# Kernel tuning notes

Measured on AMD Instinct MI355X. Metric: run time of the kernel, lower is better.

Reference implementation:

```python
import jax, jax.numpy as jnp
import numpy as np

MAX_DEG = 10  # PyG MFConv default max_degree


def mfconv(x, edge_index, W, b, Wr):
    """Degree-bucketed graph conv (PyG MFConv).
    x: [N, F_in]; edge_index: [2, E]; W, Wr: [MAX_DEG+1, F_in, F_out]; b: [MAX_DEG+1, F_out].
    out_i = lins[deg_i](sum_{j in N(i)} x_j) + root_lins[deg_i](x_i)
    """
    N = x.shape[0]
    src, dst = edge_index[0], edge_index[1]
    # sum-aggregate neighbor features (gather + scatter-add)
    h = jax.ops.segment_sum(x[src], dst, num_segments=N)  # [N, F_in]
    # in-degree per node, clamped to MAX_DEG
    deg = jax.ops.segment_sum(jnp.ones_like(dst, dtype=jnp.int32), dst, num_segments=N)
    deg = jnp.clip(deg, 0, MAX_DEG)  # [N]
    # compute all degree-bucket outputs, then select per node ([N, D+1, F_out] is small)
    out_all = jnp.einsum('nf,dfo->ndo', h, W) + b[None] + jnp.einsum('nf,dfo->ndo', x, Wr)
    return jnp.take_along_axis(out_all, deg[:, None, None], axis=1)[:, 0]  # [N, F_out]


def setup_inputs() -> dict:
    key = jax.random.key(0)
    ks = jax.random.split(key, 8)
    N, E = 100000, 1600000
    F_in, F_hid, F_out = 128, 32, 64
    D = MAX_DEG + 1
    x = jax.random.normal(ks[0], (N, F_in), dtype=jnp.float32)
    edge_index = jax.random.randint(ks[1], (2, E), 0, N, dtype=jnp.int64)
    s1 = 1.0 / np.sqrt(F_in)
    s2 = 1.0 / np.sqrt(F_hid)
    W1 = jax.random.uniform(ks[2], (D, F_in, F_hid), jnp.float32, -s1, s1)
    b1 = jax.random.uniform(ks[3], (D, F_hid), jnp.float32, -s1, s1)
    Wr1 = jax.random.uniform(ks[4], (D, F_in, F_hid), jnp.float32, -s1, s1)
    W2 = jax.random.uniform(ks[5], (D, F_hid, F_out), jnp.float32, -s2, s2)
    b2 = jax.random.uniform(ks[6], (D, F_out), jnp.float32, -s2, s2)
    Wr2 = jax.random.uniform(ks[7], (D, F_hid, F_out), jnp.float32, -s2, s2)
    return {"x": x, "edge_index": edge_index, "W1": W1, "b1": b1, "Wr1": Wr1,
            "W2": W2, "b2": b2, "Wr2": Wr2}


def reference(x, edge_index, W1, b1, Wr1, W2, b2, Wr2):
    h = mfconv(x, edge_index, W1, b1, Wr1)
    h = jax.nn.relu(h)
    return mfconv(h, edge_index, W2, b2, Wr2)
```

## Files before the change

kernel.cpp:

```cpp
#include <hip/hip_runtime.h>

#define FIN 128
#define FHID 32
#define FOUT 64
#define MAXDEG 10
#define BSH 8
#define ACHUNK 4096
#define XPAD 136
#define YPAD 40

typedef __attribute__((ext_vector_type(8))) short short8;
typedef __attribute__((ext_vector_type(4))) float f32x4;


__device__ __forceinline__ float bf2f(unsigned short u) {
    union { unsigned int i; float f; } c; c.i = ((unsigned int)u) << 16; return c.f;
}
__device__ __forceinline__ unsigned short f2bf(float f) {
    union { float f; unsigned int i; } c; c.f = f;
    unsigned int r = c.i + 0x7FFF + ((c.i >> 16) & 1);
    return (unsigned short)(r >> 16);
}
__device__ __forceinline__ float bflo(unsigned int w) { return bf2f((unsigned short)(w & 0xffff)); }
__device__ __forceinline__ float bfhi(unsigned int w) { return bf2f((unsigned short)(w >> 16)); }
__device__ __forceinline__ unsigned int pk2(float lo, float hi) {
    return (unsigned int)f2bf(lo) | ((unsigned int)f2bf(hi) << 16);
}


__global__ __launch_bounds__(256) void k_bhist(const int* __restrict__ ei, int E, int N,
                                               int* __restrict__ bcnt) {
    __shared__ int hist[1024];
    int K = ((N + 255) >> BSH);
    int t = threadIdx.x;
    long long cb = (long long)blockIdx.x * ACHUNK;
    for (int i = t; i < K; i += 256) hist[i] = 0;
    __syncthreads();
#pragma unroll
    for (int i = 0; i < 16; ++i) {
        long long e = cb + t + (long long)i * 256;
        if (e < E) {
            int ss = ei[e];
            int dd = ei[E + e];
            if ((unsigned)ss < (unsigned)N && (unsigned)dd < (unsigned)N)
                atomicAdd(&hist[dd >> BSH], 1);
        }
    }
    __syncthreads();
    for (int i = t; i < K; i += 256) {
        int h = hist[i];
        if (h) atomicAdd(&bcnt[i], h);
    }
}

__global__ __launch_bounds__(1024) void k_scanb(const int* __restrict__ bcnt, int K,
                                                int* __restrict__ bstart,
                                                int* __restrict__ gcur) {
    __shared__ int tmp[1024];
    int t = threadIdx.x;
    int v = (t < K) ? bcnt[t] : 0;
    tmp[t] = v;
    __syncthreads();
    for (int off = 1; off < 1024; off <<= 1) {
        int a = (t >= off) ? tmp[t - off] : 0;
        __syncthreads();
        tmp[t] += a;
        __syncthreads();
    }
    if (t < K) { int s = tmp[t] - v; bstart[t] = s; gcur[t] = s; }
}

__global__ __launch_bounds__(256) void k_passA(const int* __restrict__ ei, int E, int N,
                                               int* __restrict__ gcur,
                                               int2* __restrict__ pairs) {
    __shared__ int hist[1024];
    __shared__ int base[1024];
    int K = ((N + 255) >> BSH);
    int t = threadIdx.x;
    long long cb = (long long)blockIdx.x * ACHUNK;
    for (int i = t; i < K; i += 256) hist[i] = 0;
    __syncthreads();
    int sv[16], dv[16];
#pragma unroll
    for (int i = 0; i < 16; ++i) {
        sv[i] = -1; dv[i] = 0;
        long long e = cb + t + (long long)i * 256;
        if (e < E) {
            int ss = ei[e];
            int dd = ei[E + e];
            if ((unsigned)ss < (unsigned)N && (unsigned)dd < (unsigned)N) {
                sv[i] = ss; dv[i] = dd;
            }
        }
    }
#pragma unroll
    for (int i = 0; i < 16; ++i)
        if (sv[i] >= 0) atomicAdd(&hist[dv[i] >> BSH], 1);
    __syncthreads();
    for (int i = t; i < K; i += 256) {
        int h = hist[i];
        base[i] = h ? atomicAdd(&gcur[i], h) : 0;
    }
    __syncthreads();
    for (int i = t; i < K; i += 256) hist[i] = 0;
    __syncthreads();
#pragma unroll
    for (int i = 0; i < 16; ++i) {
        if (sv[i] >= 0) {
            int b = dv[i] >> BSH;
            int off = atomicAdd(&hist[b], 1);
            pairs[base[b] + off] = make_int2(sv[i], dv[i]);
        }
    }
}

__global__ __launch_bounds__(256) void k_passB2(const int2* __restrict__ pairs,
                                                const int* __restrict__ bstart,
                                                const int* __restrict__ gcur,
                                                int* __restrict__ deg,
                                                int* __restrict__ cursor,
                                                int* __restrict__ adj,
                                                int* __restrict__ nflag,
                                                int* __restrict__ flist, int N) {
    __shared__ int cnt[256];
    __shared__ int scn[256];
    __shared__ int cur[256];
    __shared__ int fids[256];
    __shared__ int fcnt, fbase;
    int b = blockIdx.x;
    int lo = b << BSH;
    int t = threadIdx.x;
    int nvalid = min(256, N - lo);
    cnt[t] = 0;
    if (t == 0) fcnt = 0;
    int pstart = bstart[b];
    int pend = gcur[b];
    __syncthreads();
    for (int i = pstart + t; i < pend; i += 256)
        atomicAdd(&cnt[pairs[i].y - lo], 1);
    __syncthreads();
    int v = cnt[t];
    scn[t] = v;
    __syncthreads();
    for (int off = 1; off < 256; off <<= 1) {
        int a = (t >= off) ? scn[t - off] : 0;
        __syncthreads();
        scn[t] += a;
        __syncthreads();
    }
    int rowstart = pstart + scn[t] - v;
    cur[t] = rowstart;
    if (t < nvalid) {
        deg[lo + t] = v;
        cursor[lo + t] = rowstart + v;
        if (v < MAXDEG) { int p = atomicAdd(&fcnt, 1); fids[p] = lo + t; }
    }
    __syncthreads();
    if (t == 0 && fcnt > 0) fbase = atomicAdd(nflag, fcnt);
    __syncthreads();
    if (t < fcnt) flist[fbase + t] = fids[t];
    for (int i = pstart + t; i < pend; i += 256) {
        int2 pr = pairs[i];
        int pos = atomicAdd(&cur[pr.y - lo], 1);
        adj[pos] = pr.x;
    }
}

__global__ __launch_bounds__(256) void k_prepack(const float* __restrict__ W1,
                                                 const float* __restrict__ Wr1,
                                                 const float* __restrict__ W2,
                                                 const float* __restrict__ Wr2,
                                                 unsigned short* __restrict__ wcat1,
                                                 unsigned short* __restrict__ wcat2) {
    int t = threadIdx.x;
    const float* W1b  = W1  + (size_t)MAXDEG * FIN * FHID;
    const float* Wr1b = Wr1 + (size_t)MAXDEG * FIN * FHID;
    const float* W2b  = W2  + (size_t)MAXDEG * FHID * FOUT;
    const float* Wr2b = Wr2 + (size_t)MAXDEG * FHID * FOUT;
    for (int i = 0; i < 32; ++i) {
        int idx = i * 256 + t;
        int n = idx >> 7, k = idx & 127;
        float v = (n < 32) ? W1b[k * FHID + n] : Wr1b[k * FHID + (n - 32)];
        wcat1[idx] = f2bf(v);
    }
    for (int i = 0; i < 16; ++i) {
        int idx = i * 256 + t;
        int n = idx >> 5, k = idx & 31;
        float v = (n < 64) ? W2b[k * FOUT + n] : Wr2b[k * FOUT + (n - 64)];
        wcat2[idx] = f2bf(v);
    }
}

__global__ __launch_bounds__(256) void k_pre1m(const float* __restrict__ x,
                                               const unsigned short* __restrict__ wcat1,
                                               const float* __restrict__ b1,
                                               unsigned short* __restrict__ z10,
                                               unsigned short* __restrict__ r1, int N) {
    __shared__ __align__(16) unsigned short xt[64 * XPAD];
    __shared__ __align__(16) unsigned short wt[64 * XPAD];
    int t = threadIdx.x;
    int row0 = blockIdx.x * 64;
    {
        const uint4* src = (const uint4*)wcat1;
#pragma unroll
        for (int i = 0; i < 4; ++i) {
            int idx = i * 256 + t;
            uint4 v = src[idx];
            int n = idx >> 4;
            int k = (idx & 15) * 8;
            *(uint4*)(wt + n * XPAD + k) = v;
        }
    }
    {
        int r = t >> 2;
        int c0 = (t & 3) * 32;
        int cr = min(row0 + r, N - 1);
        const float4* xs = (const float4*)(x + (size_t)cr * FIN + c0);
        unsigned short* dst = xt + r * XPAD + c0;
#pragma unroll
        for (int i = 0; i < 8; ++i) {
            float4 v = xs[i];
            ushort4 b;
            b.x = f2bf(v.x); b.y = f2bf(v.y); b.z = f2bf(v.z); b.w = f2bf(v.w);
            *(ushort4*)(dst + i * 4) = b;
        }
    }
    __syncthreads();
    int w = t >> 6, lane = t & 63;
    int m = lane & 15, quad = lane >> 4;
    const unsigned short* arow = xt + (w * 16 + m) * XPAD + quad * 8;
    short8 af[4];
#pragma unroll
    for (int kt = 0; kt < 4; ++kt) af[kt] = *(const short8*)(arow + kt * 32);
    f32x4 acc[4];
#pragma unroll
    for (int ct = 0; ct < 4; ++ct) acc[ct] = (f32x4){0.f, 0.f, 0.f, 0.f};
#pragma unroll
    for (int ct = 0; ct < 4; ++ct) {
        const unsigned short* brow = wt + (ct * 16 + m) * XPAD + quad * 8;
#pragma unroll
        for (int kt = 0; kt < 4; ++kt) {
            short8 bfr = *(const short8*)(brow + kt * 32);
            acc[ct] = __builtin_amdgcn_mfma_f32_16x16x32_bf16(af[kt], bfr, acc[ct], 0, 0, 0);
        }
    }
    int rbase = row0 + w * 16 + quad * 4;
#pragma unroll
    for (int ct = 0; ct < 4; ++ct) {
        float bias = (ct >= 2) ? b1[MAXDEG * FHID + (ct - 2) * 16 + m] : 0.f;
#pragma unroll
        for (int rg = 0; rg < 4; ++rg) {
            int n = rbase + rg;
            if (n < N) {
                float v = acc[ct][rg];
                if (ct < 2) z10[(size_t)n * FHID + ct * 16 + m] = f2bf(v);
                else        r1[(size_t)n * FHID + (ct - 2) * 16 + m] = f2bf(v + bias);
            }
        }
    }
}

__global__ __launch_bounds__(256) void k_fix1c(const float* __restrict__ x,
                                               const int* __restrict__ deg,
                                               const int* __restrict__ cursor,
                                               const int* __restrict__ adj,
                                               const float* __restrict__ W1,
                                               const float* __restrict__ b1,
                                               const float* __restrict__ Wr1,
                                               const int* __restrict__ nflag,
                                               const int* __restrict__ flist,
                                               unsigned short* __restrict__ out1, int N) {
    int wid = (blockIdx.x * 256 + threadIdx.x) >> 6;
    int nw = gridDim.x * 4;
    int lane = threadIdx.x & 63;
    int u = lane >> 5, o = lane & 31;
    int fcnt = *nflag;
    for (int i = wid; i < fcnt; i += nw) {
        int n = flist[i];
        int d = deg[n];
        const float* Wr = Wr1 + (size_t)d * (FIN * FHID) + o;
        const float4* xr = (const float4*)(x + (size_t)n * FIN);
        float racc = 0.f;
        for (int c = u * 16; c < u * 16 + 16; ++c) {
            float4 xv = xr[c];
            racc += xv.x * Wr[(c * 4 + 0) * FHID] + xv.y * Wr[(c * 4 + 1) * FHID]
                  + xv.z * Wr[(c * 4 + 2) * FHID] + xv.w * Wr[(c * 4 + 3) * FHID];
        }
        racc += __shfl_xor(racc, 32);
        int e1 = cursor[n];
        int e0 = e1 - d;
        float2 h = make_float2(0.f, 0.f);
        for (int k = e0; k < e1; ++k) {
            int s = adj[k];
            float2 v = *(const float2*)(x + (size_t)s * FIN + lane * 2);
            h.x += v.x; h.y += v.y;
        }
        const float* Wp = W1 + (size_t)d * (FIN * FHID) + o;
        float acc = 0.f;
        for (int f = u * 64; f < u * 64 + 64; ++f) {
            float hf = __shfl((f & 1) ? h.y : h.x, f >> 1);
            acc += hf * Wp[f * FHID];
        }
        acc += __shfl_xor(acc, 32);
        if (lane < 32) {
            float rv = racc + b1[d * FHID + o];
            out1[(size_t)n * FHID + o] = f2bf(fmaxf(acc + rv, 0.f));
        }
    }
}

__device__ __forceinline__ void gather16(const unsigned short* __restrict__ rows,
                                         const int* __restrict__ adj,
                                         int e0, int e1, int cnt, int lane,
                                         float& a0, float& a1) {
    int e = lane >> 4, f2 = lane & 15;
    int sidx = adj[min(e0 + lane, e1 - 1)];
    const unsigned short* rb = rows + f2 * 2;
    int nch = (cnt + 15) >> 4;
    for (int c = 0; c < nch; ++c) {
        int i0 = c * 16 + e;
        int i1 = i0 + 4, i2 = i0 + 8, i3 = i0 + 12;
        int s0 = __shfl(sidx, min(i0, cnt - 1));
        int s1 = __shfl(sidx, min(i1, cnt - 1));
        int s2 = __shfl(sidx, min(i2, cnt - 1));
        int s3 = __shfl(sidx, min(i3, cnt - 1));
        unsigned int w0 = *(const unsigned int*)(rb + (size_t)s0 * FHID);
        unsigned int w1 = *(const unsigned int*)(rb + (size_t)s1 * FHID);
        unsigned int w2 = *(const unsigned int*)(rb + (size_t)s2 * FHID);
        unsigned int w3 = *(const unsigned int*)(rb + (size_t)s3 * FHID);
        float c0 = (i0 < cnt) ? 1.f : 0.f;
        float c1 = (i1 < cnt) ? 1.f : 0.f;
        float c2 = (i2 < cnt) ? 1.f : 0.f;
        float c3 = (i3 < cnt) ? 1.f : 0.f;
        a0 = fmaf(c0, bflo(w0), a0); a1 = fmaf(c0, bfhi(w0), a1);
        a0 = fmaf(c1, bflo(w1), a0); a1 = fmaf(c1, bfhi(w1), a1);
        a0 = fmaf(c2, bflo(w2), a0); a1 = fmaf(c2, bfhi(w2), a1);
        a0 = fmaf(c3, bflo(w3), a0); a1 = fmaf(c3, bfhi(w3), a1);
    }
    for (int k = e0 + 64 + e; k < e1; k += 4) {
        int s = adj[k];
        unsigned int w = *(const unsigned int*)(rb + (size_t)s * FHID);
        a0 += bflo(w); a1 += bfhi(w);
    }
}

__global__ __launch_bounds__(256) void k_layer1b(const unsigned short* __restrict__ z10,
                                                 const unsigned short* __restrict__ r1,
                                                 const int* __restrict__ deg,
                                                 const int* __restrict__ cursor,
                                                 const int* __restrict__ adj,
                                                 unsigned short* __restrict__ out1, int N) {
    int wave = (int)(((long long)blockIdx.x * 256 + threadIdx.x) >> 6);
    if (wave >= N) return;
    int n = wave;
    int lane = threadIdx.x & 63;
    int dg = deg[n];
    if (dg < MAXDEG) return;
    int e1 = cursor[n];
    int e0 = e1 - dg;
    float a0 = 0.f, a1 = 0.f;
    gather16(z10, adj, e0, e1, min(dg, 64), lane, a0, a1);
    a0 += __shfl_xor(a0, 16); a1 += __shfl_xor(a1, 16);
    a0 += __shfl_xor(a0, 32); a1 += __shfl_xor(a1, 32);
    if (lane < 16) {
        int f2 = lane;
        unsigned int rv = *(const unsigned int*)(r1 + (size_t)n * FHID + f2 * 2);
        unsigned int w = pk2(fmaxf(a0 + bflo(rv), 0.f), fmaxf(a1 + bfhi(rv), 0.f));
        *(unsigned int*)(out1 + (size_t)n * FHID + f2 * 2) = w;
    }
}

__global__ __launch_bounds__(256) void k_layer2g(const unsigned short* __restrict__ y,
                                                 const int* __restrict__ deg,
                                                 const int* __restrict__ cursor,
                                                 const int* __restrict__ adj,
                                                 float* __restrict__ g, int N) {
    int wave = (int)(((long long)blockIdx.x * 256 + threadIdx.x) >> 6);
    if (wave >= N) return;
    int n = wave;
    int lane = threadIdx.x & 63;
    int dg = deg[n];
    float a0 = 0.f, a1 = 0.f;
    if (dg > 0) {
        int e1 = cursor[n];
        int e0 = e1 - dg;
        gather16(y, adj, e0, e1, min(dg, 64), lane, a0, a1);
        a0 += __shfl_xor(a0, 16); a1 += __shfl_xor(a1, 16);
        a0 += __shfl_xor(a0, 32); a1 += __shfl_xor(a1, 32);
    }
    if (lane < 16) {
        *(float2*)(g + (size_t)n * FHID + lane * 2) = make_float2(a0, a1);
    }
}

__global__ __launch_bounds__(256) void k_post2m(const float* __restrict__ g,
                                                const unsigned short* __restrict__ y,
                                                const unsigned short* __restrict__ wcat2,
                                                const float* __restrict__ b2,
                                                float* __restrict__ out, int N) {
    __shared__ __align__(16) unsigned short gt[64 * YPAD];
    __shared__ __align__(16) unsigned short yt[64 * YPAD];
    __shared__ __align__(16) unsigned short wt[128 * YPAD];
    int t = threadIdx.x;
    int row0 = blockIdx.x * 64;
    {
        const uint4* src = (const uint4*)wcat2;
#pragma unroll
        for (int i = 0; i < 2; ++i) {
            int idx = i * 256 + t;
            uint4 v = src[idx];
            int nn = idx >> 2;
            int k = (idx & 3) * 8;
            *(uint4*)(wt + nn * YPAD + k) = v;
        }
    }
    {
        int r = t >> 2, c0 = (t & 3) * 8;
        int rn = min(row0 + r, N - 1);
        const float4* gs = (const float4*)(g + (size_t)rn * FHID + c0);
        float4 v0 = gs[0], v1 = gs[1];
        ushort4 p0, p1;
        p0.x = f2bf(v0.x); p0.y = f2bf(v0.y); p0.z = f2bf(v0.z); p0.w = f2bf(v0.w);
        p1.x = f2bf(v1.x); p1.y = f2bf(v1.y); p1.z = f2bf(v1.z); p1.w = f2bf(v1.w);
        *(ushort4*)(gt + r * YPAD + c0) = p0;
        *(ushort4*)(gt + r * YPAD + c0 + 4) = p1;
        uint4 vy = *(const uint4*)(y + (size_t)rn * FHID + c0);
        *(uint4*)(yt + r * YPAD + c0) = vy;
    }
    __syncthreads();
    int w = t >> 6, lane = t & 63;
    int m = lane & 15, quad = lane >> 4;
    short8 ag = *(const short8*)(gt + (w * 16 + m) * YPAD + quad * 8);
    short8 ay = *(const short8*)(yt + (w * 16 + m) * YPAD + quad * 8);
    int rbase = row0 + w * 16 + quad * 4;
#pragma unroll
    for (int ct = 0; ct < 4; ++ct) {
        short8 bw = *(const short8*)(wt + (ct * 16 + m) * YPAD + quad * 8);
        short8 br = *(const short8*)(wt + ((64 + ct * 16) + m) * YPAD + quad * 8);
        f32x4 acc = (f32x4){0.f, 0.f, 0.f, 0.f};
        acc = __builtin_amdgcn_mfma_f32_16x16x32_bf16(ag, bw, acc, 0, 0, 0);
        acc = __builtin_amdgcn_mfma_f32_16x16x32_bf16(ay, br, acc, 0, 0, 0);
        int o = ct * 16 + m;
        float bias = b2[MAXDEG * FOUT + o];
#pragma unroll
        for (int rg = 0; rg < 4; ++rg) {
            int nn = rbase + rg;
            if (nn < N) out[(size_t)nn * FOUT + o] = acc[rg] + bias;
        }
    }
}

__global__ __launch_bounds__(256) void k_fix2c(const float* __restrict__ g,
                                               const unsigned short* __restrict__ y,
                                               const int* __restrict__ deg,
                                               const float* __restrict__ b2,
                                               const float* __restrict__ W2,
                                               const float* __restrict__ Wr2,
                                               const int* __restrict__ nflag,
                                               const int* __restrict__ flist,
                                               float* __restrict__ out, int N) {
    int wid = (blockIdx.x * 256 + threadIdx.x) >> 6;
    int nw = gridDim.x * 4;
    int lane = threadIdx.x & 63;
    int fcnt = *nflag;
    for (int i = wid; i < fcnt; i += nw) {
        int n = flist[i];
        int d = deg[n];
        const float* W2p  = W2  + (size_t)d * (FHID * FOUT) + lane;
        const float* Wr2p = Wr2 + (size_t)d * (FHID * FOUT) + lane;
        float2 gv = *(const float2*)(g + (size_t)n * FHID + (lane & 15) * 2);
        unsigned int yw = *(const unsigned int*)(y + (size_t)n * FHID + (lane & 15) * 2);
        float acc = b2[d * FOUT + lane];
#pragma unroll
        for (int q = 0; q < 16; ++q) {
            float g0 = __shfl(gv.x, q);
            float g1 = __shfl(gv.y, q);
            unsigned int yq = __shfl(yw, q);
            acc += g0 * W2p[(2 * q) * FOUT] + g1 * W2p[(2 * q + 1) * FOUT]
                 + bflo(yq) * Wr2p[(2 * q) * FOUT] + bfhi(yq) * Wr2p[(2 * q + 1) * FOUT];
        }
        out[(size_t)n * FOUT + lane] = acc;
    }
}

extern "C" void kernel_launch(void* const* d_in, const int* in_sizes, int n_in,
                              void* d_out, int out_size, void* d_ws, size_t ws_size,
                              hipStream_t stream) {
    const float* x   = (const float*)d_in[0];
    const int*   ei  = (const int*)d_in[1];
    const float* W1  = (const float*)d_in[2];
    const float* b1  = (const float*)d_in[3];
    const float* Wr1 = (const float*)d_in[4];
    const float* W2  = (const float*)d_in[5];
    const float* b2  = (const float*)d_in[6];
    const float* Wr2 = (const float*)d_in[7];

    int N = in_sizes[0] / FIN;
    int E = in_sizes[1] / 2;
    int K  = (N + 255) >> BSH;

    char* ws = (char*)d_ws;
    size_t off = 0;
    auto alloc = [&](size_t bytes) {
        void* ptr = ws + off;
        off += (bytes + 511) / 512 * 512;
        return ptr;
    };
    int* deg              = (int*)alloc((size_t)N * sizeof(int));
    int* cursor           = (int*)alloc((size_t)N * sizeof(int));
    int* bcnt             = (int*)alloc((size_t)(K + 1) * sizeof(int));
    int* nflag            = bcnt + K;
    int* bstart           = (int*)alloc((size_t)K * sizeof(int));
    int* gcur             = (int*)alloc((size_t)K * sizeof(int));
    int* flist            = (int*)alloc((size_t)N * sizeof(int));
    int* adj              = (int*)alloc((size_t)E * sizeof(int));
    unsigned short* z10   = (unsigned short*)alloc((size_t)N * FHID * 2);
    unsigned short* r1    = (unsigned short*)alloc((size_t)N * FHID * 2);
    unsigned short* out1  = (unsigned short*)alloc((size_t)N * FHID * 2);
    size_t pairsB = (size_t)E * sizeof(int2);
    size_t gB     = (size_t)N * FHID * sizeof(float);
    void* shared_region   = alloc(pairsB > gB ? pairsB : gB);
    float* g              = (float*)shared_region;
    int2* pairs           = (int2*)shared_region;
    unsigned short* wcat1 = (unsigned short*)alloc(64 * 128 * 2);
    unsigned short* wcat2 = (unsigned short*)alloc(128 * 32 * 2);

    float* out = (float*)d_out;

    hipMemsetAsync(bcnt, 0, (size_t)(K + 1) * sizeof(int), stream);

    int nwgA = (E + ACHUNK - 1) / ACHUNK;
    k_prepack<<<1, 256, 0, stream>>>(W1, Wr1, W2, Wr2, wcat1, wcat2);
    k_bhist<<<nwgA, 256, 0, stream>>>(ei, E, N, bcnt);
    k_scanb<<<1, 1024, 0, stream>>>(bcnt, K, bstart, gcur);
    k_passA<<<nwgA, 256, 0, stream>>>(ei, E, N, gcur, pairs);
    k_passB2<<<K, 256, 0, stream>>>(pairs, bstart, gcur, deg, cursor, adj, nflag, flist, N);

    int nb64 = (N + 63) / 64;
    int nb_node = (N + 3) / 4;
    int nbfix = 1024;

    k_pre1m<<<nb64, 256, 0, stream>>>(x, wcat1, b1, z10, r1, N);
    k_fix1c<<<nbfix, 256, 0, stream>>>(x, deg, cursor, adj, W1, b1, Wr1, nflag, flist, out1, N);
    k_layer1b<<<nb_node, 256, 0, stream>>>(z10, r1, deg, cursor, adj, out1, N);
    k_layer2g<<<nb_node, 256, 0, stream>>>(out1, deg, cursor, adj, g, N);
    k_post2m<<<nb64, 256, 0, stream>>>(g, out1, wcat2, b2, out, N);
    k_fix2c<<<nbfix, 256, 0, stream>>>(g, out1, deg, b2, W2, Wr2, nflag, flist, out, N);
}
```

Before: 294.2 us.

## Fuse fixup kernels into main layer kernels and pack edge pairs into 32 bits

Merges the weight prepack into the bucket-histogram kernel, and merges the low-degree fixup kernels into the layer-1 gather and layer-2 post kernels as extra blocks. This cuts the number of launches and lets both paths run concurrently. Edge pairs are packed into one 32-bit word (source index plus local destination offset), which halves the bytes written and read during the sort. The gather loop gains a fast path for full 16-edge chunks. The 20-bit source field caps N at about one million, and the layer-2 fixup now re-gathers neighbour rows instead of reading the precomputed g.

```diff
diff --git a/kernel.cpp b/kernel.cpp
--- a/kernel.cpp
+++ b/kernel.cpp
@@ -8,6 +8,7 @@
 #define ACHUNK 4096
 #define XPAD 136
 #define YPAD 40
+#define SRCBITS 20
 
 typedef __attribute__((ext_vector_type(8))) short short8;
 typedef __attribute__((ext_vector_type(4))) float f32x4;
@@ -28,8 +29,14 @@
 }
 
 
-__global__ __launch_bounds__(256) void k_bhist(const int* __restrict__ ei, int E, int N,
-                                               int* __restrict__ bcnt) {
+__global__ __launch_bounds__(256) void k_bhistp(const int* __restrict__ ei, int E, int N,
+                                                int* __restrict__ bcnt,
+                                                const float* __restrict__ W1,
+                                                const float* __restrict__ Wr1,
+                                                const float* __restrict__ W2,
+                                                const float* __restrict__ Wr2,
+                                                unsigned short* __restrict__ wcat1,
+                                                unsigned short* __restrict__ wcat2) {
     __shared__ int hist[1024];
     int K = ((N + 255) >> BSH);
     int t = threadIdx.x;
@@ -51,6 +58,24 @@
         int h = hist[i];
         if (h) atomicAdd(&bcnt[i], h);
     }
+    if (blockIdx.x == 0) {
+        const float* W1b  = W1  + (size_t)MAXDEG * FIN * FHID;
+        const float* Wr1b = Wr1 + (size_t)MAXDEG * FIN * FHID;
+        const float* W2b  = W2  + (size_t)MAXDEG * FHID * FOUT;
+        const float* Wr2b = Wr2 + (size_t)MAXDEG * FHID * FOUT;
+        for (int i = 0; i < 32; ++i) {
+            int idx = i * 256 + t;
+            int n = idx >> 7, k = idx & 127;
+            float v = (n < 32) ? W1b[k * FHID + n] : Wr1b[k * FHID + (n - 32)];
+            wcat1[idx] = f2bf(v);
+        }
+        for (int i = 0; i < 16; ++i) {
+            int idx = i * 256 + t;
+            int n = idx >> 5, k = idx & 31;
+            float v = (n < 64) ? W2b[k * FOUT + n] : Wr2b[k * FOUT + (n - 64)];
+            wcat2[idx] = f2bf(v);
+        }
+    }
 }
 
 __global__ __launch_bounds__(1024) void k_scanb(const int* __restrict__ bcnt, int K,
@@ -72,7 +97,7 @@
 
 __global__ __launch_bounds__(256) void k_passA(const int* __restrict__ ei, int E, int N,
                                                int* __restrict__ gcur,
-                                               int2* __restrict__ pairs) {
+                                               unsigned int* __restrict__ pairs) {
     __shared__ int hist[1024];
     __shared__ int base[1024];
     int K = ((N + 255) >> BSH);
@@ -109,12 +134,12 @@
         if (sv[i] >= 0) {
             int b = dv[i] >> BSH;
             int off = atomicAdd(&hist[b], 1);
-            pairs[base[b] + off] = make_int2(sv[i], dv[i]);
-        }
-    }
-}
-
-__global__ __launch_bounds__(256) void k_passB2(const int2* __restrict__ pairs,
+            pairs[base[b] + off] = (unsigned int)sv[i] | ((unsigned int)(dv[i] & 255) << SRCBITS);
+        }
+    }
+}
+
+__global__ __launch_bounds__(256) void k_passB2(const unsigned int* __restrict__ pairs,
                                                 const int* __restrict__ bstart,
                                                 const int* __restrict__ gcur,
                                                 int* __restrict__ deg,
@@ -137,7 +162,7 @@
     int pend = gcur[b];
     __syncthreads();
     for (int i = pstart + t; i < pend; i += 256)
-        atomicAdd(&cnt[pairs[i].y - lo], 1);
+        atomicAdd(&cnt[pairs[i] >> SRCBITS], 1);
     __syncthreads();
     int v = cnt[t];
     scn[t] = v;
@@ -160,34 +185,9 @@
     __syncthreads();
     if (t < fcnt) flist[fbase + t] = fids[t];
     for (int i = pstart + t; i < pend; i += 256) {
-        int2 pr = pairs[i];
-        int pos = atomicAdd(&cur[pr.y - lo], 1);
-        adj[pos] = pr.x;
-    }
-}
-
-__global__ __launch_bounds__(256) void k_prepack(const float* __restrict__ W1,
-                                                 const float* __restrict__ Wr1,
-                                                 const float* __restrict__ W2,
-                                                 const float* __restrict__ Wr2,
-                                                 unsigned short* __restrict__ wcat1,
-                                                 unsigned short* __restrict__ wcat2) {
-    int t = threadIdx.x;
-    const float* W1b  = W1  + (size_t)MAXDEG * FIN * FHID;
-    const float* Wr1b = Wr1 + (size_t)MAXDEG * FIN * FHID;
-    const float* W2b  = W2  + (size_t)MAXDEG * FHID * FOUT;
-    const float* Wr2b = Wr2 + (size_t)MAXDEG * FHID * FOUT;
-    for (int i = 0; i < 32; ++i) {
-        int idx = i * 256 + t;
-        int n = idx >> 7, k = idx & 127;
-        float v = (n < 32) ? W1b[k * FHID + n] : Wr1b[k * FHID + (n - 32)];
-        wcat1[idx] = f2bf(v);
-    }
-    for (int i = 0; i < 16; ++i) {
-        int idx = i * 256 + t;
-        int n = idx >> 5, k = idx & 31;
-        float v = (n < 64) ? W2b[k * FOUT + n] : Wr2b[k * FOUT + (n - 64)];
-        wcat2[idx] = f2bf(v);
+        unsigned int pr = pairs[i];
+        int pos = atomicAdd(&cur[pr >> SRCBITS], 1);
+        adj[pos] = (int)(pr & ((1u << SRCBITS) - 1));
     }
 }
 
@@ -260,55 +260,6 @@
     }
 }
 
-__global__ __launch_bounds__(256) void k_fix1c(const float* __restrict__ x,
-                                               const int* __restrict__ deg,
-                                               const int* __restrict__ cursor,
-                                               const int* __restrict__ adj,
-                                               const float* __restrict__ W1,
-                                               const float* __restrict__ b1,
-                                               const float* __restrict__ Wr1,
-                                               const int* __restrict__ nflag,
-                                               const int* __restrict__ flist,
-                                               unsigned short* __restrict__ out1, int N) {
-    int wid = (blockIdx.x * 256 + threadIdx.x) >> 6;
-    int nw = gridDim.x * 4;
-    int lane = threadIdx.x & 63;
-    int u = lane >> 5, o = lane & 31;
-    int fcnt = *nflag;
-    for (int i = wid; i < fcnt; i += nw) {
-        int n = flist[i];
-        int d = deg[n];
-        const float* Wr = Wr1 + (size_t)d * (FIN * FHID) + o;
-        const float4* xr = (const float4*)(x + (size_t)n * FIN);
-        float racc = 0.f;
-        for (int c = u * 16; c < u * 16 + 16; ++c) {
-            float4 xv = xr[c];
-            racc += xv.x * Wr[(c * 4 + 0) * FHID] + xv.y * Wr[(c * 4 + 1) * FHID]
-                  + xv.z * Wr[(c * 4 + 2) * FHID] + xv.w * Wr[(c * 4 + 3) * FHID];
-        }
-        racc += __shfl_xor(racc, 32);
-        int e1 = cursor[n];
-        int e0 = e1 - d;
-        float2 h = make_float2(0.f, 0.f);
-        for (int k = e0; k < e1; ++k) {
-            int s = adj[k];
-            float2 v = *(const float2*)(x + (size_t)s * FIN + lane * 2);
-            h.x += v.x; h.y += v.y;
-        }
-        const float* Wp = W1 + (size_t)d * (FIN * FHID) + o;
-        float acc = 0.f;
-        for (int f = u * 64; f < u * 64 + 64; ++f) {
-            float hf = __shfl((f & 1) ? h.y : h.x, f >> 1);
-            acc += hf * Wp[f * FHID];
-        }
-        acc += __shfl_xor(acc, 32);
-        if (lane < 32) {
-            float rv = racc + b1[d * FHID + o];
-            out1[(size_t)n * FHID + o] = f2bf(fmaxf(acc + rv, 0.f));
-        }
-    }
-}
-
 __device__ __forceinline__ void gather16(const unsigned short* __restrict__ rows,
                                          const int* __restrict__ adj,
                                          int e0, int e1, int cnt, int lane,
@@ -316,9 +267,24 @@
     int e = lane >> 4, f2 = lane & 15;
     int sidx = adj[min(e0 + lane, e1 - 1)];
     const unsigned short* rb = rows + f2 * 2;
-    int nch = (cnt + 15) >> 4;
-    for (int c = 0; c < nch; ++c) {
+    int nfull = cnt >> 4;
+    for (int c = 0; c < nfull; ++c) {
         int i0 = c * 16 + e;
+        int s0 = __shfl(sidx, i0);
+        int s1 = __shfl(sidx, i0 + 4);
+        int s2 = __shfl(sidx, i0 + 8);
+        int s3 = __shfl(sidx, i0 + 12);
+        unsigned int w0 = *(const unsigned int*)(rb + (size_t)s0 * FHID);
+        unsigned int w1 = *(const unsigned int*)(rb + (size_t)s1 * FHID);
+        unsigned int w2 = *(const unsigned int*)(rb + (size_t)s2 * FHID);
+        unsigned int w3 = *(const unsigned int*)(rb + (size_t)s3 * FHID);
+        a0 += bflo(w0); a1 += bfhi(w0);
+        a0 += bflo(w1); a1 += bfhi(w1);
+        a0 += bflo(w2); a1 += bfhi(w2);
+        a0 += bflo(w3); a1 += bfhi(w3);
+    }
+    if (cnt & 15) {
+        int i0 = nfull * 16 + e;
         int i1 = i0 + 4, i2 = i0 + 8, i3 = i0 + 12;
         int s0 = __shfl(sidx, min(i0, cnt - 1));
         int s1 = __shfl(sidx, min(i1, cnt - 1));
@@ -344,29 +310,74 @@
     }
 }
 
-__global__ __launch_bounds__(256) void k_layer1b(const unsigned short* __restrict__ z10,
+__global__ __launch_bounds__(256) void k_layer1x(const unsigned short* __restrict__ z10,
                                                  const unsigned short* __restrict__ r1,
                                                  const int* __restrict__ deg,
                                                  const int* __restrict__ cursor,
                                                  const int* __restrict__ adj,
-                                                 unsigned short* __restrict__ out1, int N) {
-    int wave = (int)(((long long)blockIdx.x * 256 + threadIdx.x) >> 6);
-    if (wave >= N) return;
-    int n = wave;
-    int lane = threadIdx.x & 63;
-    int dg = deg[n];
-    if (dg < MAXDEG) return;
-    int e1 = cursor[n];
-    int e0 = e1 - dg;
-    float a0 = 0.f, a1 = 0.f;
-    gather16(z10, adj, e0, e1, min(dg, 64), lane, a0, a1);
-    a0 += __shfl_xor(a0, 16); a1 += __shfl_xor(a1, 16);
-    a0 += __shfl_xor(a0, 32); a1 += __shfl_xor(a1, 32);
-    if (lane < 16) {
-        int f2 = lane;
-        unsigned int rv = *(const unsigned int*)(r1 + (size_t)n * FHID + f2 * 2);
-        unsigned int w = pk2(fmaxf(a0 + bflo(rv), 0.f), fmaxf(a1 + bfhi(rv), 0.f));
-        *(unsigned int*)(out1 + (size_t)n * FHID + f2 * 2) = w;
+                                                 const float* __restrict__ x,
+                                                 const float* __restrict__ W1,
+                                                 const float* __restrict__ b1,
+                                                 const float* __restrict__ Wr1,
+                                                 const int* __restrict__ nflag,
+                                                 const int* __restrict__ flist,
+                                                 unsigned short* __restrict__ out1,
+                                                 int N, int nbFast) {
+    int t = threadIdx.x;
+    int lane = t & 63;
+    if ((int)blockIdx.x < nbFast) {
+        int n = blockIdx.x * 4 + (t >> 6);
+        if (n >= N) return;
+        int dg = deg[n];
+        if (dg < MAXDEG) return;
+        int e1 = cursor[n];
+        int e0 = e1 - dg;
+        float a0 = 0.f, a1 = 0.f;
+        gather16(z10, adj, e0, e1, min(dg, 64), lane, a0, a1);
+        a0 += __shfl_xor(a0, 16); a1 += __shfl_xor(a1, 16);
+        a0 += __shfl_xor(a0, 32); a1 += __shfl_xor(a1, 32);
+        if (lane < 16) {
+            unsigned int rv = *(const unsigned int*)(r1 + (size_t)n * FHID + lane * 2);
+            unsigned int w = pk2(fmaxf(a0 + bflo(rv), 0.f), fmaxf(a1 + bfhi(rv), 0.f));
+            *(unsigned int*)(out1 + (size_t)n * FHID + lane * 2) = w;
+        }
+    } else {
+        int wid = ((blockIdx.x - nbFast) * 256 + t) >> 6;
+        int nw = (gridDim.x - nbFast) * 4;
+        int u = lane >> 5, o = lane & 31;
+        int fcnt = *nflag;
+        for (int i = wid; i < fcnt; i += nw) {
+            int n = flist[i];
+            int d = deg[n];
+            const float* Wr = Wr1 + (size_t)d * (FIN * FHID) + o;
+            const float4* xr = (const float4*)(x + (size_t)n * FIN);
+            float racc = 0.f;
+            for (int c = u * 16; c < u * 16 + 16; ++c) {
+                float4 xv = xr[c];
+                racc += xv.x * Wr[(c * 4 + 0) * FHID] + xv.y * Wr[(c * 4 + 1) * FHID]
+                      + xv.z * Wr[(c * 4 + 2) * FHID] + xv.w * Wr[(c * 4 + 3) * FHID];
+            }
+            racc += __shfl_xor(racc, 32);
+            int e1 = cursor[n];
+            int e0 = e1 - d;
+            float2 h = make_float2(0.f, 0.f);
+            for (int k = e0; k < e1; ++k) {
+                int s = adj[k];
+                float2 v = *(const float2*)(x + (size_t)s * FIN + lane * 2);
+                h.x += v.x; h.y += v.y;
+            }
+            const float* Wp = W1 + (size_t)d * (FIN * FHID) + o;
+            float acc = 0.f;
+            for (int f = u * 64; f < u * 64 + 64; ++f) {
+                float hf = __shfl((f & 1) ? h.y : h.x, f >> 1);
+                acc += hf * Wp[f * FHID];
+            }
+            acc += __shfl_xor(acc, 32);
+            if (lane < 32) {
+                float rv = racc + b1[d * FHID + o];
+                out1[(size_t)n * FHID + o] = f2bf(fmaxf(acc + rv, 0.f));
+            }
+        }
     }
 }
 
@@ -393,93 +404,105 @@
     }
 }
 
-__global__ __launch_bounds__(256) void k_post2m(const float* __restrict__ g,
+__global__ __launch_bounds__(256) void k_post2x(const float* __restrict__ g,
                                                 const unsigned short* __restrict__ y,
                                                 const unsigned short* __restrict__ wcat2,
                                                 const float* __restrict__ b2,
-                                                float* __restrict__ out, int N) {
-    __shared__ __align__(16) unsigned short gt[64 * YPAD];
-    __shared__ __align__(16) unsigned short yt[64 * YPAD];
-    __shared__ __align__(16) unsigned short wt[128 * YPAD];
-    int t = threadIdx.x;
-    int row0 = blockIdx.x * 64;
-    {
-        const uint4* src = (const uint4*)wcat2;
-#pragma unroll
-        for (int i = 0; i < 2; ++i) {
-            int idx = i * 256 + t;
-            uint4 v = src[idx];
-            int nn = idx >> 2;
-            int k = (idx & 3) * 8;
-            *(uint4*)(wt + nn * YPAD + k) = v;
-        }
-    }
-    {
-        int r = t >> 2, c0 = (t & 3) * 8;
-        int rn = min(row0 + r, N - 1);
-        const float4* gs = (const float4*)(g + (size_t)rn * FHID + c0);
-        float4 v0 = gs[0], v1 = gs[1];
-        ushort4 p0, p1;
-        p0.x = f2bf(v0.x); p0.y = f2bf(v0.y); p0.z = f2bf(v0.z); p0.w = f2bf(v0.w);
-        p1.x = f2bf(v1.x); p1.y = f2bf(v1.y); p1.z = f2bf(v1.z); p1.w = f2bf(v1.w);
-        *(ushort4*)(gt + r * YPAD + c0) = p0;
-        *(ushort4*)(gt + r * YPAD + c0 + 4) = p1;
-        uint4 vy = *(const uint4*)(y + (size_t)rn * FHID + c0);
-        *(uint4*)(yt + r * YPAD + c0) = vy;
-    }
-    __syncthreads();
-    int w = t >> 6, lane = t & 63;
-    int m = lane & 15, quad = lane >> 4;
-    short8 ag = *(const short8*)(gt + (w * 16 + m) * YPAD + quad * 8);
-    short8 ay = *(const short8*)(yt + (w * 16 + m) * YPAD + quad * 8);
-    int rbase = row0 + w * 16 + quad * 4;
-#pragma unroll
-    for (int ct = 0; ct < 4; ++ct) {
-        short8 bw = *(const short8*)(wt + (ct * 16 + m) * YPAD + quad * 8);
-        short8 br = *(const short8*)(wt + ((64 + ct * 16) + m) * YPAD + quad * 8);
-        f32x4 acc = (f32x4){0.f, 0.f, 0.f, 0.f};
-        acc = __builtin_amdgcn_mfma_f32_16x16x32_bf16(ag, bw, acc, 0, 0, 0);
-        acc = __builtin_amdgcn_mfma_f32_16x16x32_bf16(ay, br, acc, 0, 0, 0);
-        int o = ct * 16 + m;
-        float bias = b2[MAXDEG * FOUT + o];
-#pragma unroll
-        for (int rg = 0; rg < 4; ++rg) {
-            int nn = rbase + rg;
-            if (nn < N) out[(size_t)nn * FOUT + o] = acc[rg] + bias;
-        }
-    }
-}
-
-__global__ __launch_bounds__(256) void k_fix2c(const float* __restrict__ g,
-                                               const unsigned short* __restrict__ y,
-                                               const int* __restrict__ deg,
-                                               const float* __restrict__ b2,
-                                               const float* __restrict__ W2,
-                                               const float* __restrict__ Wr2,
-                                               const int* __restrict__ nflag,
-                                               const int* __restrict__ flist,
-                                               float* __restrict__ out, int N) {
-    int wid = (blockIdx.x * 256 + threadIdx.x) >> 6;
-    int nw = gridDim.x * 4;
-    int lane = threadIdx.x & 63;
-    int fcnt = *nflag;
-    for (int i = wid; i < fcnt; i += nw) {
-        int n = flist[i];
-        int d = deg[n];
-        const float* W2p  = W2  + (size_t)d * (FHID * FOUT) + lane;
-        const float* Wr2p = Wr2 + (size_t)d * (FHID * FOUT) + lane;
-        float2 gv = *(const float2*)(g + (size_t)n * FHID + (lane & 15) * 2);
-        unsigned int yw = *(const unsigned int*)(y + (size_t)n * FHID + (lane & 15) * 2);
-        float acc = b2[d * FOUT + lane];
-#pragma unroll
-        for (int q = 0; q < 16; ++q) {
-            float g0 = __shfl(gv.x, q);
-            float g1 = __shfl(gv.y, q);
-            unsigned int yq = __shfl(yw, q);
-            acc += g0 * W2p[(2 * q) * FOUT] + g1 * W2p[(2 * q + 1) * FOUT]
-                 + bflo(yq) * Wr2p[(2 * q) * FOUT] + bfhi(yq) * Wr2p[(2 * q + 1) * FOUT];
-        }
-        out[(size_t)n * FOUT + lane] = acc;
+                                                const int* __restrict__ deg,
+                                                const int* __restrict__ cursor,
+                                                const int* __restrict__ adj,
+                                                const float* __restrict__ W2full,
+                                                const float* __restrict__ Wr2full,
+                                                const int* __restrict__ nflag,
+                                                const int* __restrict__ flist,
+                                                float* __restrict__ out,
+                                                int N, int nbFast) {
+    int t = threadIdx.x;
+    if ((int)blockIdx.x < nbFast) {
+        __shared__ __align__(16) unsigned short gt[64 * YPAD];
+        __shared__ __align__(16) unsigned short yt[64 * YPAD];
+        __shared__ __align__(16) unsigned short wt[128 * YPAD];
+        __shared__ unsigned char flg[64];
+        int row0 = blockIdx.x * 64;
+        {
+            const uint4* src = (const uint4*)wcat2;
+#pragma unroll
+            for (int i = 0; i < 2; ++i) {
+                int idx = i * 256 + t;
+                uint4 v = src[idx];
+                int nn = idx >> 2;
+                int k = (idx & 3) * 8;
+                *(uint4*)(wt + nn * YPAD + k) = v;
+            }
+        }
+        if (t < 64) {
+            int rn = row0 + t;
+            flg[t] = (rn < N) ? (unsigned char)(deg[rn] < MAXDEG) : (unsigned char)1;
+        }
+        {
+            int r = t >> 2, c0 = (t & 3) * 8;
+            int rn = min(row0 + r, N - 1);
+            const float4* gs = (const float4*)(g + (size_t)rn * FHID + c0);
+            float4 v0 = gs[0], v1 = gs[1];
+            ushort4 p0, p1;
+            p0.x = f2bf(v0.x); p0.y = f2bf(v0.y); p0.z = f2bf(v0.z); p0.w = f2bf(v0.w);
+            p1.x = f2bf(v1.x); p1.y = f2bf(v1.y); p1.z = f2bf(v1.z); p1.w = f2bf(v1.w);
+            *(ushort4*)(gt + r * YPAD + c0) = p0;
+            *(ushort4*)(gt + r * YPAD + c0 + 4) = p1;
+            uint4 vy = *(const uint4*)(y + (size_t)rn * FHID + c0);
+            *(uint4*)(yt + r * YPAD + c0) = vy;
+        }
+        __syncthreads();
+        int w = t >> 6, lane = t & 63;
+        int m = lane & 15, quad = lane >> 4;
+        short8 ag = *(const short8*)(gt + (w * 16 + m) * YPAD + quad * 8);
+        short8 ay = *(const short8*)(yt + (w * 16 + m) * YPAD + quad * 8);
+        int rbase = w * 16 + quad * 4;
+#pragma unroll
+        for (int ct = 0; ct < 4; ++ct) {
+            short8 bw = *(const short8*)(wt + (ct * 16 + m) * YPAD + quad * 8);
+            short8 br = *(const short8*)(wt + ((64 + ct * 16) + m) * YPAD + quad * 8);
+            f32x4 acc = (f32x4){0.f, 0.f, 0.f, 0.f};
+            acc = __builtin_amdgcn_mfma_f32_16x16x32_bf16(ag, bw, acc, 0, 0, 0);
+            acc = __builtin_amdgcn_mfma_f32_16x16x32_bf16(ay, br, acc, 0, 0, 0);
+            int o = ct * 16 + m;
+            float bias = b2[MAXDEG * FOUT + o];
+#pragma unroll
+            for (int rg = 0; rg < 4; ++rg) {
+                int rl = rbase + rg;
+                int nn = row0 + rl;
+                if (nn < N && !flg[rl]) out[(size_t)nn * FOUT + o] = acc[rg] + bias;
+            }
+        }
+    } else {
+        int wid = ((blockIdx.x - nbFast) * 256 + t) >> 6;
+        int nw = (gridDim.x - nbFast) * 4;
+        int lane = t & 63;
+        int fcnt = *nflag;
+        for (int i = wid; i < fcnt; i += nw) {
+            int n = flist[i];
+            int d = deg[n];
+            float a0 = 0.f, a1 = 0.f;
+            if (d > 0) {
+                int e1 = cursor[n];
+                gather16(y, adj, e1 - d, e1, d, lane, a0, a1);
+                a0 += __shfl_xor(a0, 16); a1 += __shfl_xor(a1, 16);
+                a0 += __shfl_xor(a0, 32); a1 += __shfl_xor(a1, 32);
+            }
+            const float* W2p  = W2full  + (size_t)d * (FHID * FOUT) + lane;
+            const float* Wr2p = Wr2full + (size_t)d * (FHID * FOUT) + lane;
+            unsigned int yw = *(const unsigned int*)(y + (size_t)n * FHID + (lane & 15) * 2);
+            float acc = b2[d * FOUT + lane];
+#pragma unroll
+            for (int q = 0; q < 16; ++q) {
+                float g0 = __shfl(a0, q);
+                float g1 = __shfl(a1, q);
+                unsigned int yq = __shfl(yw, q);
+                acc += g0 * W2p[(2 * q) * FOUT] + g1 * W2p[(2 * q + 1) * FOUT]
+                     + bflo(yq) * Wr2p[(2 * q) * FOUT] + bfhi(yq) * Wr2p[(2 * q + 1) * FOUT];
+            }
+            out[(size_t)n * FOUT + lane] = acc;
+        }
     }
 }
 
@@ -517,33 +540,33 @@
     unsigned short* z10   = (unsigned short*)alloc((size_t)N * FHID * 2);
     unsigned short* r1    = (unsigned short*)alloc((size_t)N * FHID * 2);
     unsigned short* out1  = (unsigned short*)alloc((size_t)N * FHID * 2);
-    size_t pairsB = (size_t)E * sizeof(int2);
+    size_t pairsB = (size_t)E * sizeof(unsigned int);
     size_t gB     = (size_t)N * FHID * sizeof(float);
     void* shared_region   = alloc(pairsB > gB ? pairsB : gB);
     float* g              = (float*)shared_region;
-    int2* pairs           = (int2*)shared_region;
+    unsigned int* pairs   = (unsigned int*)shared_region;
     unsigned short* wcat1 = (unsigned short*)alloc(64 * 128 * 2);
     unsigned short* wcat2 = (unsigned short*)alloc(128 * 32 * 2);
 
     float* out = (float*)d_out;
 
-    hipMemsetAsync(bcnt, 0, (size_t)(K + 1) * sizeof(int), stream);
+    (void)hipMemsetAsync(bcnt, 0, (size_t)(K + 1) * sizeof(int), stream);
 
     int nwgA = (E + ACHUNK - 1) / ACHUNK;
-    k_prepack<<<1, 256, 0, stream>>>(W1, Wr1, W2, Wr2, wcat1, wcat2);
-    k_bhist<<<nwgA, 256, 0, stream>>>(ei, E, N, bcnt);
+    k_bhistp<<<nwgA, 256, 0, stream>>>(ei, E, N, bcnt, W1, Wr1, W2, Wr2, wcat1, wcat2);
     k_scanb<<<1, 1024, 0, stream>>>(bcnt, K, bstart, gcur);
     k_passA<<<nwgA, 256, 0, stream>>>(ei, E, N, gcur, pairs);
     k_passB2<<<K, 256, 0, stream>>>(pairs, bstart, gcur, deg, cursor, adj, nflag, flist, N);
 
     int nb64 = (N + 63) / 64;
     int nb_node = (N + 3) / 4;
-    int nbfix = 1024;
+    const int FIXB = 512;
 
     k_pre1m<<<nb64, 256, 0, stream>>>(x, wcat1, b1, z10, r1, N);
-    k_fix1c<<<nbfix, 256, 0, stream>>>(x, deg, cursor, adj, W1, b1, Wr1, nflag, flist, out1, N);
-    k_layer1b<<<nb_node, 256, 0, stream>>>(z10, r1, deg, cursor, adj, out1, N);
+    k_layer1x<<<nb_node + FIXB, 256, 0, stream>>>(z10, r1, deg, cursor, adj,
+                                                  x, W1, b1, Wr1, nflag, flist, out1,
+                                                  N, nb_node);
     k_layer2g<<<nb_node, 256, 0, stream>>>(out1, deg, cursor, adj, g, N);
-    k_post2m<<<nb64, 256, 0, stream>>>(g, out1, wcat2, b2, out, N);
-    k_fix2c<<<nbfix, 256, 0, stream>>>(g, out1, deg, b2, W2, Wr2, nflag, flist, out, N);
-}
+    k_post2x<<<nb64 + FIXB, 256, 0, stream>>>(g, out1, wcat2, b2, deg, cursor, adj,
+                                              W2, Wr2, nflag, flist, out, N, nb64);
+}
```

Result: faster. 287.5 us (-2.3%).
